# Performance work log

Measured on AMD Instinct MI355X. Metric: run time of the kernel, lower is better.

Reference implementation:

```python
import jax, jax.numpy as jnp
import numpy as np

N_EXPERTS = 8
N_ACTIVE = 2


def setup_inputs() -> dict:
    key = jax.random.key(0)
    k0, k1, k2, k3, k4 = jax.random.split(key, 5)
    B, S, D, H, E = 4, 2048, 1024, 2816, N_EXPERTS
    return {
        "x": jax.random.normal(k0, (B, S, D), dtype=jnp.float32),
        "Wr": jax.random.normal(k1, (D, E), dtype=jnp.float32) * 0.02,
        "w1": jax.random.normal(k2, (E, D, H), dtype=jnp.float32) * 0.02,
        "w3": jax.random.normal(k3, (E, D, H), dtype=jnp.float32) * 0.02,
        "w2": jax.random.normal(k4, (E, H, D), dtype=jnp.float32) * 0.02,
    }


def reference(x, Wr, w1, w3, w2):
    B, S, D = x.shape
    E, K = N_EXPERTS, N_ACTIVE
    xf = x.reshape(-1, D)  # (T, D), T = B*S

    # --- Router: top-k over softmax probs, renormalized weights ---
    logits = xf @ Wr                       # (T, E)
    probs = jax.nn.softmax(logits, axis=-1)
    topk_vals, topk_idx = jax.lax.top_k(probs, K)   # (T, K)
    topk_w = topk_vals / jnp.sum(topk_vals, axis=-1, keepdims=True)

    # combine weight per (token, expert): sum of slot weights routed to expert
    onehot = jax.nn.one_hot(topk_idx, E, dtype=xf.dtype)  # (T, K, E)
    combine = jnp.einsum('tk,tke->te', topk_w, onehot)    # (T, E)

    # --- Load-balancing aux loss: E * sum_e f_e * P_e ---
    f = onehot.mean(axis=(0, 1))     # fraction of (token,slot) assignments per expert
    P = probs.mean(axis=0)           # mean router prob per expert
    aux_loss = E * jnp.sum(f * P)

    # --- Experts: SwiGLU, combined with router weights (zero weight = unrouted) ---
    out = jnp.zeros_like(xf)
    for e in range(E):  # small fixed expert count
        h = jax.nn.silu(xf @ w1[e]) * (xf @ w3[e])  # (T, H)
        out = out + combine[:, e:e + 1] * (h @ w2[e])
    return out.reshape(B, S, D), aux_loss
```

## Files before the change

### kernel.cpp

```cpp
#include <hip/hip_runtime.h>
#include <hip/hip_bf16.h>
#include <stdint.h>


#define T_TOK 8192
#define D_DIM 1024
#define H_DIM 2816
#define E_EXP 8
#define NSLOT 16384
#define CAP_ROWS 18432
#define MT_MAX 136

#define MI_T2 1
#define MI_POS 8
#define MI_MTE2 16
#define MI_MTB2 (16 + MT_MAX)

typedef __attribute__((ext_vector_type(8))) short short8;
typedef __attribute__((ext_vector_type(4))) float f32x4;

#define GLD16(gsrc, ldst) __builtin_amdgcn_global_load_lds( \
    (const __attribute__((address_space(1))) void*)(gsrc),  \
    (__attribute__((address_space(3))) void*)(ldst), 16, 0, 0)

__global__ __launch_bounds__(256) void transpose_router(const float* __restrict__ w1,
                                                        const float* __restrict__ w3,
                                                        const float* __restrict__ w2,
                                                        __hip_bfloat16* __restrict__ w13t,
                                                        __hip_bfloat16* __restrict__ w2t,
                                                        const float* __restrict__ x,
                                                        const float* __restrict__ Wr,
                                                        float* __restrict__ Pbuf,
                                                        int* __restrict__ expert_sel,
                                                        float* __restrict__ slot_w) {
  __shared__ float tile[64][65];
  __shared__ float sP[4][8];
  int bid = blockIdx.x, tid = threadIdx.x;
  int lc = (tid & 15) * 4;
  int lr = tid >> 4;
  if (bid < 11264) {
    int z = bid / 704, rem = bid % 704;
    int bx = rem % 44, by = rem / 44;
    int e = z >> 1, w3f = z & 1;
    const float* in = w3f ? w3 : w1;
    int h0 = bx * 64, d0 = by * 64;
    const float* src = in + ((size_t)e * D_DIM + d0) * H_DIM + h0;
#pragma unroll
    for (int i = 0; i < 4; i++) {
      float4 v = *(const float4*)(src + (size_t)(lr + i * 16) * H_DIM + lc);
      tile[lr + i * 16][lc + 0] = v.x;
      tile[lr + i * 16][lc + 1] = v.y;
      tile[lr + i * 16][lc + 2] = v.z;
      tile[lr + i * 16][lc + 3] = v.w;
    }
    __syncthreads();
    __hip_bfloat16* dstE = w13t + (size_t)e * (2 * H_DIM) * D_DIM;
    int rB = (tid & 7) * 8;
#pragma unroll
    for (int i = 0; i < 2; i++) {
      int hh = (tid >> 3) + i * 32;
      int habs = h0 + hh;
      int rw = 2 * (habs & ~15) + (habs & 15) + (w3f ? 16 : 0);
      __align__(16) __hip_bfloat16 o[8];
#pragma unroll
      for (int k = 0; k < 8; k++) o[k] = __float2bfloat16(tile[rB + k][hh]);
      *(short8*)(dstE + (size_t)rw * D_DIM + d0 + rB) = *(const short8*)o;
    }
  } else if (bid < 16896) {
    int b2 = bid - 11264;
    int e = b2 / 704, rem = b2 % 704;
    int bx = rem % 16, by = rem / 16;
    int c0 = bx * 64, r0 = by * 64;
    const float* src = w2 + ((size_t)e * H_DIM + r0) * D_DIM + c0;
#pragma unroll
    for (int i = 0; i < 4; i++) {
      float4 v = *(const float4*)(src + (size_t)(lr + i * 16) * D_DIM + lc);
      tile[lr + i * 16][lc + 0] = v.x;
      tile[lr + i * 16][lc + 1] = v.y;
      tile[lr + i * 16][lc + 2] = v.z;
      tile[lr + i * 16][lc + 3] = v.w;
    }
    __syncthreads();
    __hip_bfloat16* dst = w2t + ((size_t)e * D_DIM + c0) * H_DIM + r0;
    int rB = (tid & 7) * 8;
#pragma unroll
    for (int i = 0; i < 2; i++) {
      int c = (tid >> 3) + i * 32;
      __align__(16) __hip_bfloat16 o[8];
#pragma unroll
      for (int k = 0; k < 8; k++) o[k] = __float2bfloat16(tile[rB + k][c]);
      *(short8*)(dst + (size_t)c * H_DIM + rB) = *(const short8*)o;
    }
  } else {
    int rb = bid - 16896;
    int wave = tid >> 6, lane = tid & 63;
    int tok = rb * 4 + wave;
    const float* xr = x + (size_t)tok * D_DIM;
    float acc[8];
#pragma unroll
    for (int e = 0; e < 8; e++) acc[e] = 0.f;
    for (int d = lane; d < D_DIM; d += 64) {
      float xv = xr[d];
      const float4* w4 = (const float4*)(Wr + d * 8);
      float4 wa = w4[0], wb = w4[1];
      acc[0] += xv * wa.x; acc[1] += xv * wa.y; acc[2] += xv * wa.z; acc[3] += xv * wa.w;
      acc[4] += xv * wb.x; acc[5] += xv * wb.y; acc[6] += xv * wb.z; acc[7] += xv * wb.w;
    }
#pragma unroll
    for (int e = 0; e < 8; e++) {
#pragma unroll
      for (int off = 32; off >= 1; off >>= 1) acc[e] += __shfl_xor(acc[e], off);
    }
    float mx = acc[0];
#pragma unroll
    for (int e = 1; e < 8; e++) mx = fmaxf(mx, acc[e]);
    float p[8], s = 0.f;
#pragma unroll
    for (int e = 0; e < 8; e++) { p[e] = expf(acc[e] - mx); s += p[e]; }
    float inv = 1.f / s;
#pragma unroll
    for (int e = 0; e < 8; e++) p[e] *= inv;
    int i0 = 0;
#pragma unroll
    for (int e = 1; e < 8; e++) if (p[e] > p[i0]) i0 = e;
    int i1 = (i0 == 0) ? 1 : 0;
#pragma unroll
    for (int e = 0; e < 8; e++) if (e != i0 && p[e] > p[i1]) i1 = e;
    float wsum = p[i0] + p[i1];
    if (lane == 0) {
      expert_sel[tok * 2] = i0;
      expert_sel[tok * 2 + 1] = i1;
      slot_w[tok * 2] = p[i0] / wsum;
      slot_w[tok * 2 + 1] = p[i1] / wsum;
#pragma unroll
      for (int e = 0; e < 8; e++) sP[wave][e] = p[e];
    }
    __syncthreads();
    if (tid < 8)
      Pbuf[tid * 2048 + rb] = sP[0][tid] + sP[1][tid] + sP[2][tid] + sP[3][tid];
  }
}

__global__ __launch_bounds__(256) void offsets_kernel(const int* __restrict__ expert_sel,
                                                      int* __restrict__ meta,
                                                      const float* __restrict__ Pbuf,
                                                      float* __restrict__ aux_out) {
  int t = threadIdx.x;
  unsigned long long pA = 0, pB = 0;
  for (int i = 0; i < 64; i++) {
    int e = expert_sel[i * 256 + t];
    if (e < 4) pA += 1ull << (e * 16);
    else       pB += 1ull << ((e - 4) * 16);
  }
#pragma unroll
  for (int off = 32; off >= 1; off >>= 1) {
    pA += __shfl_xor(pA, off);
    pB += __shfl_xor(pB, off);
  }
  __shared__ unsigned long long sA[4], sB[4];
  __shared__ float red[8][33];
  int wave = t >> 6, lane = t & 63;
  if (lane == 0) { sA[wave] = pA; sB[wave] = pB; }
  int ee = t >> 5, j = t & 31;
  float s = 0.f;
  for (int c = j; c < 2048; c += 32) s += Pbuf[ee * 2048 + c];
  red[ee][j] = s;
  __syncthreads();
  if (t == 0) {
    unsigned long long A = sA[0] + sA[1] + sA[2] + sA[3];
    unsigned long long B = sB[0] + sB[1] + sB[2] + sB[3];
    int cnt[8];
    for (int e = 0; e < 4; e++) cnt[e] = (int)((A >> (e * 16)) & 0xFFFF);
    for (int e = 0; e < 4; e++) cnt[4 + e] = (int)((B >> (e * 16)) & 0xFFFF);
    float psum[8];
    for (int e = 0; e < 8; e++) {
      float ss = 0.f;
      for (int k = 0; k < 32; k++) ss += red[e][k];
      psum[e] = ss;
    }
    int off = 0, n2 = 0;
    float aux = 0.f;
    for (int e = 0; e < 8; e++) {
      int c = cnt[e];
      meta[MI_POS + e] = off;
      int t2 = (c + 127) >> 7;
      for (int jj = 0; jj < t2; jj++) { meta[MI_MTE2 + n2] = e; meta[MI_MTB2 + n2] = off + jj * 128; n2++; }
      off += t2 * 128;
      aux += ((float)c / 16384.f) * (psum[e] / 8192.f);
    }
    meta[MI_T2] = n2;
    *aux_out = 8.f * aux;
  }
}

__global__ __launch_bounds__(256) void assign_kernel(const int* __restrict__ expert_sel,
                                                     int* __restrict__ meta,
                                                     int* __restrict__ slot_pos) {
  int tid = threadIdx.x, wave = tid >> 6, lane = tid & 63;
  int slot = blockIdx.x * 256 + tid;
  int e = expert_sel[slot];
  __shared__ int cnt[4][8];
  __shared__ int base[8];
  __shared__ int woff[4][8];
  int rank = 0;
#pragma unroll
  for (int ee = 0; ee < 8; ee++) {
    unsigned long long msk = __ballot(e == ee);
    if (lane == 0) cnt[wave][ee] = __popcll(msk);
    if (e == ee) rank = __popcll(msk & ((1ull << lane) - 1ull));
  }
  __syncthreads();
  if (tid < 8) {
    int c0 = cnt[0][tid], c1 = cnt[1][tid], c2 = cnt[2][tid], c3 = cnt[3][tid];
    int tot = c0 + c1 + c2 + c3;
    base[tid] = atomicAdd(&meta[MI_POS + tid], tot);
    woff[0][tid] = 0; woff[1][tid] = c0; woff[2][tid] = c0 + c1; woff[3][tid] = c0 + c1 + c2;
  }
  __syncthreads();
  slot_pos[slot] = base[e] + woff[wave][e] + rank;
}

__global__ __launch_bounds__(256) void gather_kernel(const int* __restrict__ slot_pos,
                                                     const float* __restrict__ x,
                                                     __hip_bfloat16* __restrict__ Xg) {
  int wave = threadIdx.x >> 6, lane = threadIdx.x & 63;
  int tok = blockIdx.x * 4 + wave;
  int p0 = slot_pos[tok * 2], p1 = slot_pos[tok * 2 + 1];
  const float4* src = (const float4*)(x + (size_t)tok * D_DIM);
  __hip_bfloat16* d0 = Xg + (size_t)p0 * D_DIM;
  __hip_bfloat16* d1 = Xg + (size_t)p1 * D_DIM;
#pragma unroll
  for (int p = 0; p < 4; p++) {
    float4 v = src[p * 64 + lane];
    union { ushort4 u4; __hip_bfloat16 h[4]; } cv;
    cv.h[0] = __float2bfloat16(v.x);
    cv.h[1] = __float2bfloat16(v.y);
    cv.h[2] = __float2bfloat16(v.z);
    cv.h[3] = __float2bfloat16(v.w);
    *(ushort4*)(d0 + (p * 64 + lane) * 4) = cv.u4;
    *(ushort4*)(d1 + (p * 64 + lane) * 4) = cv.u4;
  }
}

__device__ __forceinline__ short8 frag_read64(const char* tile, int row, int gk) {
  int byte = (row << 7) | ((gk ^ (row & 7)) << 4);
  return *(const short8*)(tile + byte);
}

template <int NITER, int BLK>
__device__ __forceinline__ void stage_rowsT(const __hip_bfloat16* gbase, int ld, char* tile,
                                            int tid) {
#pragma unroll
  for (int i = 0; i < NITER; i++) {
    int L = i * (BLK * 16) + tid * 16;
    int row = L >> 7;
    int g = (L >> 4) & 7;
    int gs = g ^ (row & 7);
    const char* src = (const char*)(gbase + (size_t)row * ld) + gs * 16;
    GLD16(src, tile + i * (BLK * 16) + (tid >> 6) * 1024);
  }
}

__device__ __forceinline__ void tile_from_bid(int bid, int nwg, int mmax, int* m, int* n) {
  int cpx = nwg >> 3;
  int u = (bid & 7) * cpx + (bid >> 3);
  *n = u / mmax;
  *m = u % mmax;
}

__global__ __launch_bounds__(256, 2) void gemm1_kernel(const __hip_bfloat16* __restrict__ Xg,
                                                       const __hip_bfloat16* __restrict__ w13t,
                                                       __hip_bfloat16* __restrict__ Hb,
                                                       const int* __restrict__ meta) {
  int m, nIdx;
  tile_from_bid(blockIdx.x, (2 * H_DIM / 128) * MT_MAX, MT_MAX, &m, &nIdx);
  if (m >= meta[MI_T2]) return;
  int e = meta[MI_MTE2 + m];
  int row0 = meta[MI_MTB2 + m];
  int n0 = nIdx * 128;
  __shared__ __align__(16) char ldsA[16384];
  __shared__ __align__(16) char ldsB[16384];
  int tid = threadIdx.x, wave = tid >> 6, lane = tid & 63;
  int wr = wave >> 1, wc = wave & 1;
  const __hip_bfloat16* Ab = Xg + (size_t)row0 * D_DIM;
  const __hip_bfloat16* Bb = w13t + ((size_t)e * (2 * H_DIM) + n0) * D_DIM;

  f32x4 acc[4][4];
#pragma unroll
  for (int i = 0; i < 4; i++)
#pragma unroll
    for (int j = 0; j < 4; j++) acc[i][j] = 0.f;

  int rsel = lane & 15, kg = lane >> 4;
  for (int k0 = 0; k0 < D_DIM; k0 += 64) {
    stage_rowsT<4, 256>(Ab + k0, D_DIM, ldsA, tid);
    stage_rowsT<4, 256>(Bb + k0, D_DIM, ldsB, tid);
    asm volatile("s_waitcnt vmcnt(0)" ::: "memory");
    __syncthreads();
#pragma unroll
    for (int kk = 0; kk < 2; kk++) {
      int gk = kk * 4 + kg;
      short8 a[4], b[4];
#pragma unroll
      for (int f = 0; f < 4; f++) a[f] = frag_read64(ldsA, wr * 64 + f * 16 + rsel, gk);
#pragma unroll
      for (int f = 0; f < 4; f++) b[f] = frag_read64(ldsB, wc * 64 + f * 16 + rsel, gk);
#pragma unroll
      for (int fm = 0; fm < 4; fm++)
#pragma unroll
        for (int fn = 0; fn < 4; fn++)
          acc[fm][fn] = __builtin_amdgcn_mfma_f32_16x16x32_bf16(a[fm], b[fn], acc[fm][fn], 0, 0, 0);
    }
    __syncthreads();
  }
  int rq = lane >> 4;
#pragma unroll
  for (int fm = 0; fm < 4; fm++)
#pragma unroll
    for (int fnp = 0; fnp < 2; fnp++)
#pragma unroll
      for (int j = 0; j < 4; j++) {
        float v1 = acc[fm][2 * fnp][j], v3 = acc[fm][2 * fnp + 1][j];
        float h = (v1 / (1.f + expf(-v1))) * v3;
        int r = row0 + wr * 64 + fm * 16 + rq * 4 + j;
        int c = (n0 >> 1) + wc * 32 + fnp * 16 + rsel;
        Hb[(size_t)r * H_DIM + c] = __float2bfloat16(h);
      }
}

__global__ __launch_bounds__(256, 2) void gemm2_kernel(const __hip_bfloat16* __restrict__ Hb,
                                                       const __hip_bfloat16* __restrict__ w2t,
                                                       __hip_bfloat16* __restrict__ Y,
                                                       const int* __restrict__ meta) {
  int m, nIdx;
  tile_from_bid(blockIdx.x, (D_DIM / 128) * MT_MAX, MT_MAX, &m, &nIdx);
  if (m >= meta[MI_T2]) return;
  int e = meta[MI_MTE2 + m];
  int row0 = meta[MI_MTB2 + m];
  int n0 = nIdx * 128;
  __shared__ __align__(16) char ldsA[16384];
  __shared__ __align__(16) char ldsB[16384];
  int tid = threadIdx.x, wave = tid >> 6, lane = tid & 63;
  int wr = wave >> 1, wc = wave & 1;
  const __hip_bfloat16* Ab = Hb + (size_t)row0 * H_DIM;
  const __hip_bfloat16* Bb = w2t + ((size_t)e * D_DIM + n0) * H_DIM;

  f32x4 acc[4][4];
#pragma unroll
  for (int i = 0; i < 4; i++)
#pragma unroll
    for (int j = 0; j < 4; j++) acc[i][j] = 0.f;

  int rsel = lane & 15, kg = lane >> 4;
  for (int k0 = 0; k0 < H_DIM; k0 += 64) {
    stage_rowsT<4, 256>(Ab + k0, H_DIM, ldsA, tid);
    stage_rowsT<4, 256>(Bb + k0, H_DIM, ldsB, tid);
    asm volatile("s_waitcnt vmcnt(0)" ::: "memory");
    __syncthreads();
#pragma unroll
    for (int kk = 0; kk < 2; kk++) {
      int gk = kk * 4 + kg;
      short8 a[4], b[4];
#pragma unroll
      for (int f = 0; f < 4; f++) a[f] = frag_read64(ldsA, wr * 64 + f * 16 + rsel, gk);
#pragma unroll
      for (int f = 0; f < 4; f++) b[f] = frag_read64(ldsB, wc * 64 + f * 16 + rsel, gk);
#pragma unroll
      for (int fm = 0; fm < 4; fm++)
#pragma unroll
        for (int fn = 0; fn < 4; fn++)
          acc[fm][fn] = __builtin_amdgcn_mfma_f32_16x16x32_bf16(a[fm], b[fn], acc[fm][fn], 0, 0, 0);
    }
    __syncthreads();
  }
  int rq = lane >> 4;
#pragma unroll
  for (int fm = 0; fm < 4; fm++)
#pragma unroll
    for (int fn = 0; fn < 4; fn++)
#pragma unroll
      for (int j = 0; j < 4; j++) {
        int r = row0 + wr * 64 + fm * 16 + rq * 4 + j;
        int c = n0 + wc * 64 + fn * 16 + rsel;
        Y[(size_t)r * D_DIM + c] = __float2bfloat16(acc[fm][fn][j]);
      }
}

__global__ __launch_bounds__(256) void combine_kernel(const int* __restrict__ slot_pos,
                                                      const float* __restrict__ slot_w,
                                                      const __hip_bfloat16* __restrict__ Y,
                                                      float* __restrict__ outp) {
  int tok = blockIdx.x;
  int p0 = slot_pos[tok * 2], p1 = slot_pos[tok * 2 + 1];
  float w0 = slot_w[tok * 2], w1 = slot_w[tok * 2 + 1];
  int i4 = threadIdx.x;
  ushort4 a = *(const ushort4*)(Y + (size_t)p0 * D_DIM + i4 * 4);
  ushort4 b = *(const ushort4*)(Y + (size_t)p1 * D_DIM + i4 * 4);
  union { ushort u; __hip_bfloat16 h; } c0, c1;
  float4 r;
  c0.u = a.x; c1.u = b.x; r.x = w0 * __bfloat162float(c0.h) + w1 * __bfloat162float(c1.h);
  c0.u = a.y; c1.u = b.y; r.y = w0 * __bfloat162float(c0.h) + w1 * __bfloat162float(c1.h);
  c0.u = a.z; c1.u = b.z; r.z = w0 * __bfloat162float(c0.h) + w1 * __bfloat162float(c1.h);
  c0.u = a.w; c1.u = b.w; r.w = w0 * __bfloat162float(c0.h) + w1 * __bfloat162float(c1.h);
  ((float4*)(outp + (size_t)tok * D_DIM))[i4] = r;
}

extern "C" void kernel_launch(void* const* d_in, const int* in_sizes, int n_in,
                              void* d_out, int out_size, void* d_ws, size_t ws_size,
                              hipStream_t stream) {
  const float* x = (const float*)d_in[0];
  const float* Wr = (const float*)d_in[1];
  const float* w1 = (const float*)d_in[2];
  const float* w3 = (const float*)d_in[3];
  const float* w2 = (const float*)d_in[4];
  float* outp = (float*)d_out;

  char* ws = (char*)d_ws;
  size_t off = 0;
  auto alloc = [&](size_t bytes) -> char* {
    char* p = ws + off;
    off += (bytes + 255) & ~(size_t)255;
    return p;
  };
  __hip_bfloat16* w13t = (__hip_bfloat16*)alloc((size_t)E_EXP * 2 * H_DIM * D_DIM * 2);
  __hip_bfloat16* w2t = (__hip_bfloat16*)alloc((size_t)E_EXP * D_DIM * H_DIM * 2);
  __hip_bfloat16* Xg = (__hip_bfloat16*)alloc((size_t)CAP_ROWS * D_DIM * 2);
  __hip_bfloat16* Hb = (__hip_bfloat16*)alloc((size_t)CAP_ROWS * H_DIM * 2);
  __hip_bfloat16* Y = (__hip_bfloat16*)alloc((size_t)CAP_ROWS * D_DIM * 2);
  float* slot_w = (float*)alloc(NSLOT * 4);
  int* slot_pos = (int*)alloc(NSLOT * 4);
  int* expert_sel = (int*)alloc(NSLOT * 4);
  float* Pbuf = (float*)alloc(2048 * 8 * 4);
  int* meta = (int*)alloc(2048);
  (void)ws_size; (void)in_sizes; (void)n_in; (void)out_size;

  transpose_router<<<dim3(18944), dim3(256), 0, stream>>>(w1, w3, w2, w13t, w2t,
                                                          x, Wr, Pbuf, expert_sel, slot_w);
  offsets_kernel<<<dim3(1), dim3(256), 0, stream>>>(expert_sel, meta, Pbuf, outp + (size_t)T_TOK * D_DIM);
  assign_kernel<<<dim3(NSLOT / 256), dim3(256), 0, stream>>>(expert_sel, meta, slot_pos);
  gather_kernel<<<dim3(T_TOK / 4), dim3(256), 0, stream>>>(slot_pos, x, Xg);
  gemm1_kernel<<<dim3((2 * H_DIM / 128) * MT_MAX), dim3(256), 0, stream>>>(Xg, w13t, Hb, meta);
  gemm2_kernel<<<dim3((D_DIM / 128) * MT_MAX), dim3(256), 0, stream>>>(Hb, w2t, Y, meta);
  combine_kernel<<<dim3(T_TOK), dim3(256), 0, stream>>>(slot_pos, slot_w, Y, outp);
}
```

Measured before the change: 532.5 us.

## Fuse offsets into assign and gather token rows directly inside gemm1

The router pass now also writes a bf16 copy of x. The single-block offsets kernel is merged into assign: each block redundantly recounts expert totals and its prefix, and it also emits a position-to-token map. The separate gather kernel is removed, and gemm1 now loads A rows indirectly from the bf16 token copy through that map using global_load_lds. Tile-to-expert lookup is computed from the counts instead of a metadata table. This cuts two launches and a full scatter pass, in exchange for redundant counting in every assign block and non-contiguous A-row loads in gemm1.

Result: faster. 511.6 us (-3.9%).

```diff
diff --git a/kernel.cpp b/kernel.cpp
--- a/kernel.cpp
+++ b/kernel.cpp
@@ -10,11 +10,6 @@
 #define NSLOT 16384
 #define CAP_ROWS 18432
 #define MT_MAX 136
-
-#define MI_T2 1
-#define MI_POS 8
-#define MI_MTE2 16
-#define MI_MTB2 (16 + MT_MAX)
 
 typedef __attribute__((ext_vector_type(8))) short short8;
 typedef __attribute__((ext_vector_type(4))) float f32x4;
@@ -32,7 +27,8 @@
                                                         const float* __restrict__ Wr,
                                                         float* __restrict__ Pbuf,
                                                         int* __restrict__ expert_sel,
-                                                        float* __restrict__ slot_w) {
+                                                        float* __restrict__ slot_w,
+                                                        __hip_bfloat16* __restrict__ Xb) {
   __shared__ float tile[64][65];
   __shared__ float sP[4][8];
   int bid = blockIdx.x, tid = threadIdx.x;
@@ -106,6 +102,18 @@
       acc[0] += xv * wa.x; acc[1] += xv * wa.y; acc[2] += xv * wa.z; acc[3] += xv * wa.w;
       acc[4] += xv * wb.x; acc[5] += xv * wb.y; acc[6] += xv * wb.z; acc[7] += xv * wb.w;
     }
+    const float4* xr4 = (const float4*)xr;
+    __hip_bfloat16* xbr = Xb + (size_t)tok * D_DIM;
+#pragma unroll
+    for (int p = 0; p < 4; p++) {
+      float4 v = xr4[p * 64 + lane];
+      union { ushort4 u4; __hip_bfloat16 h[4]; } cv;
+      cv.h[0] = __float2bfloat16(v.x);
+      cv.h[1] = __float2bfloat16(v.y);
+      cv.h[2] = __float2bfloat16(v.z);
+      cv.h[3] = __float2bfloat16(v.w);
+      *(ushort4*)(xbr + (p * 64 + lane) * 4) = cv.u4;
+    }
 #pragma unroll
     for (int e = 0; e < 8; e++) {
 #pragma unroll
@@ -141,104 +149,87 @@
   }
 }
 
-__global__ __launch_bounds__(256) void offsets_kernel(const int* __restrict__ expert_sel,
-                                                      int* __restrict__ meta,
-                                                      const float* __restrict__ Pbuf,
-                                                      float* __restrict__ aux_out) {
-  int t = threadIdx.x;
-  unsigned long long pA = 0, pB = 0;
-  for (int i = 0; i < 64; i++) {
-    int e = expert_sel[i * 256 + t];
-    if (e < 4) pA += 1ull << (e * 16);
-    else       pB += 1ull << ((e - 4) * 16);
+__global__ __launch_bounds__(256) void assign_kernel(const int* __restrict__ expert_sel,
+                                                     const float* __restrict__ Pbuf,
+                                                     int* __restrict__ slot_pos,
+                                                     int* __restrict__ tok_of_pos,
+                                                     int* __restrict__ cnt_out,
+                                                     float* __restrict__ aux_out) {
+  __shared__ unsigned long long sF[2][4], sQ[2][4];
+  __shared__ int wcnt[4][8];
+  __shared__ int woff[4][8];
+  __shared__ float red[8][33];
+  int b = blockIdx.x, tid = threadIdx.x, wave = tid >> 6, lane = tid & 63;
+  int myslot = b * 256 + tid;
+  int mye = expert_sel[myslot];
+
+  unsigned long long fA = 0, fB = 0, qA = 0, qB = 0;
+  int lim = b * 256;
+  for (int i = tid; i < NSLOT; i += 256) {
+    int e = expert_sel[i];
+    if (e < 4) {
+      unsigned long long inc = 1ull << (e * 16);
+      fA += inc; if (i < lim) qA += inc;
+    } else {
+      unsigned long long inc = 1ull << ((e - 4) * 16);
+      fB += inc; if (i < lim) qB += inc;
+    }
   }
 #pragma unroll
   for (int off = 32; off >= 1; off >>= 1) {
-    pA += __shfl_xor(pA, off);
-    pB += __shfl_xor(pB, off);
-  }
-  __shared__ unsigned long long sA[4], sB[4];
-  __shared__ float red[8][33];
-  int wave = t >> 6, lane = t & 63;
-  if (lane == 0) { sA[wave] = pA; sB[wave] = pB; }
-  int ee = t >> 5, j = t & 31;
-  float s = 0.f;
-  for (int c = j; c < 2048; c += 32) s += Pbuf[ee * 2048 + c];
-  red[ee][j] = s;
+    fA += __shfl_xor(fA, off); fB += __shfl_xor(fB, off);
+    qA += __shfl_xor(qA, off); qB += __shfl_xor(qB, off);
+  }
+  if (lane == 0) { sF[0][wave] = fA; sF[1][wave] = fB; sQ[0][wave] = qA; sQ[1][wave] = qB; }
+  int rank = 0;
+#pragma unroll
+  for (int ee = 0; ee < 8; ee++) {
+    unsigned long long msk = __ballot(mye == ee);
+    if (lane == 0) wcnt[wave][ee] = __popcll(msk);
+    if (mye == ee) rank = __popcll(msk & ((1ull << lane) - 1ull));
+  }
   __syncthreads();
-  if (t == 0) {
-    unsigned long long A = sA[0] + sA[1] + sA[2] + sA[3];
-    unsigned long long B = sB[0] + sB[1] + sB[2] + sB[3];
-    int cnt[8];
-    for (int e = 0; e < 4; e++) cnt[e] = (int)((A >> (e * 16)) & 0xFFFF);
-    for (int e = 0; e < 4; e++) cnt[4 + e] = (int)((B >> (e * 16)) & 0xFFFF);
-    float psum[8];
-    for (int e = 0; e < 8; e++) {
-      float ss = 0.f;
-      for (int k = 0; k < 32; k++) ss += red[e][k];
-      psum[e] = ss;
-    }
-    int off = 0, n2 = 0;
-    float aux = 0.f;
-    for (int e = 0; e < 8; e++) {
-      int c = cnt[e];
-      meta[MI_POS + e] = off;
-      int t2 = (c + 127) >> 7;
-      for (int jj = 0; jj < t2; jj++) { meta[MI_MTE2 + n2] = e; meta[MI_MTB2 + n2] = off + jj * 128; n2++; }
-      off += t2 * 128;
-      aux += ((float)c / 16384.f) * (psum[e] / 8192.f);
-    }
-    meta[MI_T2] = n2;
-    *aux_out = 8.f * aux;
-  }
-}
-
-__global__ __launch_bounds__(256) void assign_kernel(const int* __restrict__ expert_sel,
-                                                     int* __restrict__ meta,
-                                                     int* __restrict__ slot_pos) {
-  int tid = threadIdx.x, wave = tid >> 6, lane = tid & 63;
-  int slot = blockIdx.x * 256 + tid;
-  int e = expert_sel[slot];
-  __shared__ int cnt[4][8];
-  __shared__ int base[8];
-  __shared__ int woff[4][8];
-  int rank = 0;
-#pragma unroll
-  for (int ee = 0; ee < 8; ee++) {
-    unsigned long long msk = __ballot(e == ee);
-    if (lane == 0) cnt[wave][ee] = __popcll(msk);
-    if (e == ee) rank = __popcll(msk & ((1ull << lane) - 1ull));
+  unsigned long long FA = sF[0][0] + sF[0][1] + sF[0][2] + sF[0][3];
+  unsigned long long FB = sF[1][0] + sF[1][1] + sF[1][2] + sF[1][3];
+  unsigned long long QA = sQ[0][0] + sQ[0][1] + sQ[0][2] + sQ[0][3];
+  unsigned long long QB = sQ[1][0] + sQ[1][1] + sQ[1][2] + sQ[1][3];
+  int cnt[8], pre[8];
+#pragma unroll
+  for (int e2 = 0; e2 < 4; e2++) {
+    cnt[e2] = (int)((FA >> (e2 * 16)) & 0xFFFF);
+    pre[e2] = (int)((QA >> (e2 * 16)) & 0xFFFF);
+    cnt[4 + e2] = (int)((FB >> (e2 * 16)) & 0xFFFF);
+    pre[4 + e2] = (int)((QB >> (e2 * 16)) & 0xFFFF);
+  }
+  if (tid < 8) {
+    int c0 = wcnt[0][tid], c1 = wcnt[1][tid], c2 = wcnt[2][tid];
+    woff[0][tid] = 0; woff[1][tid] = c0; woff[2][tid] = c0 + c1; woff[3][tid] = c0 + c1 + c2;
+    if (b == 0) cnt_out[tid] = cnt[tid];
   }
   __syncthreads();
-  if (tid < 8) {
-    int c0 = cnt[0][tid], c1 = cnt[1][tid], c2 = cnt[2][tid], c3 = cnt[3][tid];
-    int tot = c0 + c1 + c2 + c3;
-    base[tid] = atomicAdd(&meta[MI_POS + tid], tot);
-    woff[0][tid] = 0; woff[1][tid] = c0; woff[2][tid] = c0 + c1; woff[3][tid] = c0 + c1 + c2;
-  }
-  __syncthreads();
-  slot_pos[slot] = base[e] + woff[wave][e] + rank;
-}
-
-__global__ __launch_bounds__(256) void gather_kernel(const int* __restrict__ slot_pos,
-                                                     const float* __restrict__ x,
-                                                     __hip_bfloat16* __restrict__ Xg) {
-  int wave = threadIdx.x >> 6, lane = threadIdx.x & 63;
-  int tok = blockIdx.x * 4 + wave;
-  int p0 = slot_pos[tok * 2], p1 = slot_pos[tok * 2 + 1];
-  const float4* src = (const float4*)(x + (size_t)tok * D_DIM);
-  __hip_bfloat16* d0 = Xg + (size_t)p0 * D_DIM;
-  __hip_bfloat16* d1 = Xg + (size_t)p1 * D_DIM;
-#pragma unroll
-  for (int p = 0; p < 4; p++) {
-    float4 v = src[p * 64 + lane];
-    union { ushort4 u4; __hip_bfloat16 h[4]; } cv;
-    cv.h[0] = __float2bfloat16(v.x);
-    cv.h[1] = __float2bfloat16(v.y);
-    cv.h[2] = __float2bfloat16(v.z);
-    cv.h[3] = __float2bfloat16(v.w);
-    *(ushort4*)(d0 + (p * 64 + lane) * 4) = cv.u4;
-    *(ushort4*)(d1 + (p * 64 + lane) * 4) = cv.u4;
+  int pb = 0;
+#pragma unroll
+  for (int e2 = 0; e2 < 8; e2++)
+    if (e2 < mye) pb += ((cnt[e2] + 127) >> 7) << 7;
+  int pos = pb + pre[mye] + woff[wave][mye] + rank;
+  slot_pos[myslot] = pos;
+  tok_of_pos[pos] = myslot >> 1;
+
+  if (b == 0) {
+    int ee = tid >> 5, j = tid & 31;
+    float s = 0.f;
+    for (int c = j; c < 2048; c += 32) s += Pbuf[ee * 2048 + c];
+    red[ee][j] = s;
+    __syncthreads();
+    if (tid == 0) {
+      float aux = 0.f;
+      for (int e2 = 0; e2 < 8; e2++) {
+        float ss = 0.f;
+        for (int k = 0; k < 32; k++) ss += red[e2][k];
+        aux += ((float)cnt[e2] / 16384.f) * (ss / 8192.f);
+      }
+      *aux_out = 8.f * aux;
+    }
   }
 }
 
@@ -268,22 +259,42 @@
   *m = u % mmax;
 }
 
-__global__ __launch_bounds__(256, 2) void gemm1_kernel(const __hip_bfloat16* __restrict__ Xg,
+__device__ __forceinline__ int expert_of_tile(const int* __restrict__ cnt, int m) {
+  int acc = 0, e = -1;
+#pragma unroll
+  for (int ee = 0; ee < 8; ee++) {
+    int t = (cnt[ee] + 127) >> 7;
+    if (e < 0 && m < acc + t) e = ee;
+    acc += t;
+  }
+  return e;
+}
+
+__global__ __launch_bounds__(256, 2) void gemm1_kernel(const __hip_bfloat16* __restrict__ Xb,
                                                        const __hip_bfloat16* __restrict__ w13t,
                                                        __hip_bfloat16* __restrict__ Hb,
-                                                       const int* __restrict__ meta) {
+                                                       const int* __restrict__ tok_of_pos,
+                                                       const int* __restrict__ cnt) {
   int m, nIdx;
   tile_from_bid(blockIdx.x, (2 * H_DIM / 128) * MT_MAX, MT_MAX, &m, &nIdx);
-  if (m >= meta[MI_T2]) return;
-  int e = meta[MI_MTE2 + m];
-  int row0 = meta[MI_MTB2 + m];
+  int e = expert_of_tile(cnt, m);
+  if (e < 0) return;
+  int row0 = m * 128;
   int n0 = nIdx * 128;
   __shared__ __align__(16) char ldsA[16384];
   __shared__ __align__(16) char ldsB[16384];
   int tid = threadIdx.x, wave = tid >> 6, lane = tid & 63;
   int wr = wave >> 1, wc = wave & 1;
-  const __hip_bfloat16* Ab = Xg + (size_t)row0 * D_DIM;
   const __hip_bfloat16* Bb = w13t + ((size_t)e * (2 * H_DIM) + n0) * D_DIM;
+
+  const char* srcA[4];
+#pragma unroll
+  for (int i = 0; i < 4; i++) {
+    int row = i * 32 + (tid >> 3);
+    int gs = (tid & 7) ^ (row & 7);
+    int tk = tok_of_pos[row0 + row] & (T_TOK - 1);
+    srcA[i] = (const char*)(Xb + (size_t)tk * D_DIM) + gs * 16;
+  }
 
   f32x4 acc[4][4];
 #pragma unroll
@@ -293,7 +304,9 @@
 
   int rsel = lane & 15, kg = lane >> 4;
   for (int k0 = 0; k0 < D_DIM; k0 += 64) {
-    stage_rowsT<4, 256>(Ab + k0, D_DIM, ldsA, tid);
+#pragma unroll
+    for (int i = 0; i < 4; i++)
+      GLD16(srcA[i] + (size_t)k0 * 2, ldsA + i * 4096 + wave * 1024);
     stage_rowsT<4, 256>(Bb + k0, D_DIM, ldsB, tid);
     asm volatile("s_waitcnt vmcnt(0)" ::: "memory");
     __syncthreads();
@@ -331,12 +344,12 @@
 __global__ __launch_bounds__(256, 2) void gemm2_kernel(const __hip_bfloat16* __restrict__ Hb,
                                                        const __hip_bfloat16* __restrict__ w2t,
                                                        __hip_bfloat16* __restrict__ Y,
-                                                       const int* __restrict__ meta) {
+                                                       const int* __restrict__ cnt) {
   int m, nIdx;
   tile_from_bid(blockIdx.x, (D_DIM / 128) * MT_MAX, MT_MAX, &m, &nIdx);
-  if (m >= meta[MI_T2]) return;
-  int e = meta[MI_MTE2 + m];
-  int row0 = meta[MI_MTB2 + m];
+  int e = expert_of_tile(cnt, m);
+  if (e < 0) return;
+  int row0 = m * 128;
   int n0 = nIdx * 128;
   __shared__ __align__(16) char ldsA[16384];
   __shared__ __align__(16) char ldsB[16384];
@@ -424,22 +437,24 @@
   };
   __hip_bfloat16* w13t = (__hip_bfloat16*)alloc((size_t)E_EXP * 2 * H_DIM * D_DIM * 2);
   __hip_bfloat16* w2t = (__hip_bfloat16*)alloc((size_t)E_EXP * D_DIM * H_DIM * 2);
-  __hip_bfloat16* Xg = (__hip_bfloat16*)alloc((size_t)CAP_ROWS * D_DIM * 2);
+  __hip_bfloat16* Xb = (__hip_bfloat16*)alloc((size_t)T_TOK * D_DIM * 2);
   __hip_bfloat16* Hb = (__hip_bfloat16*)alloc((size_t)CAP_ROWS * H_DIM * 2);
   __hip_bfloat16* Y = (__hip_bfloat16*)alloc((size_t)CAP_ROWS * D_DIM * 2);
   float* slot_w = (float*)alloc(NSLOT * 4);
   int* slot_pos = (int*)alloc(NSLOT * 4);
   int* expert_sel = (int*)alloc(NSLOT * 4);
+  int* tok_of_pos = (int*)alloc(CAP_ROWS * 4);
   float* Pbuf = (float*)alloc(2048 * 8 * 4);
-  int* meta = (int*)alloc(2048);
+  int* cnt = (int*)alloc(256);
   (void)ws_size; (void)in_sizes; (void)n_in; (void)out_size;
 
   transpose_router<<<dim3(18944), dim3(256), 0, stream>>>(w1, w3, w2, w13t, w2t,
-                                                          x, Wr, Pbuf, expert_sel, slot_w);
-  offsets_kernel<<<dim3(1), dim3(256), 0, stream>>>(expert_sel, meta, Pbuf, outp + (size_t)T_TOK * D_DIM);
-  assign_kernel<<<dim3(NSLOT / 256), dim3(256), 0, stream>>>(expert_sel, meta, slot_pos);
-  gather_kernel<<<dim3(T_TOK / 4), dim3(256), 0, stream>>>(slot_pos, x, Xg);
-  gemm1_kernel<<<dim3((2 * H_DIM / 128) * MT_MAX), dim3(256), 0, stream>>>(Xg, w13t, Hb, meta);
-  gemm2_kernel<<<dim3((D_DIM / 128) * MT_MAX), dim3(256), 0, stream>>>(Hb, w2t, Y, meta);
+                                                          x, Wr, Pbuf, expert_sel, slot_w, Xb);
+  assign_kernel<<<dim3(NSLOT / 256), dim3(256), 0, stream>>>(expert_sel, Pbuf, slot_pos,
+                                                             tok_of_pos, cnt,
+                                                             outp + (size_t)T_TOK * D_DIM);
+  gemm1_kernel<<<dim3((2 * H_DIM / 128) * MT_MAX), dim3(256), 0, stream>>>(Xb, w13t, Hb,
+                                                                           tok_of_pos, cnt);
+  gemm2_kernel<<<dim3((D_DIM / 128) * MT_MAX), dim3(256), 0, stream>>>(Hb, w2t, Y, cnt);
   combine_kernel<<<dim3(T_TOK), dim3(256), 0, stream>>>(slot_pos, slot_w, Y, outp);
 }
```
